# Optimization experiments

Hardware: AMD Instinct MI355X
Metric: run time of the kernel (lower is better)

Reference implementation:

```python
import jax, jax.numpy as jnp
import numpy as np

H = 16        # num heads
NOPE = 128    # qk_nope_head_dim
ROPE = 64     # qk_rope_head_dim
VD = 128      # v_head_dim
HID = 2048    # hidden_dim
QLR = 1536    # q_lora_rank
KVLR = 512    # kv_lora_rank
B = 4
S = 1024
EPS = 1e-6


def setup_inputs() -> dict:
    key = jax.random.key(0)
    ks = jax.random.split(key, 8)
    def w(k, o, i):
        return jax.random.normal(k, (o, i), jnp.float32) * 0.02
    x = jax.random.normal(ks[0], (B * S, HID), jnp.float32)
    wq_a = w(ks[1], QLR, HID)
    w_qa_ln = jnp.ones((QLR,), jnp.float32)
    wq_b = w(ks[2], H * (NOPE + ROPE), QLR)
    wkv_a = w(ks[3], KVLR + ROPE, HID)
    w_kva_ln = jnp.ones((KVLR,), jnp.float32)
    wk_b = w(ks[4], H * NOPE, KVLR)
    wv_b = w(ks[5], H * VD, KVLR)
    wo = w(ks[6], HID, H * VD)
    # interleaved RoPE tables: [S, ROPE//2]
    pos = jnp.arange(S, dtype=jnp.float32)
    inv_freq = 1.0 / (10000.0 ** (jnp.arange(0, ROPE, 2, dtype=jnp.float32) / ROPE))
    freqs = pos[:, None] * inv_freq[None, :]
    rotary_sin = jnp.sin(freqs)
    rotary_cos = jnp.cos(freqs)
    seqstarts = jnp.arange(B + 1, dtype=jnp.int32) * S
    return dict(x=x, wq_a=wq_a, w_qa_ln=w_qa_ln, wq_b=wq_b, wkv_a=wkv_a,
                w_kva_ln=w_kva_ln, wk_b=wk_b, wv_b=wv_b, wo=wo,
                rotary_sin=rotary_sin, rotary_cos=rotary_cos, seqstarts=seqstarts)


def rmsnorm(h, w):
    return h * jax.lax.rsqrt(jnp.mean(h * h, axis=-1, keepdims=True) + EPS) * w


def rope_interleaved(t, sin, cos):
    # t: [B,S,h,ROPE]; sin/cos: [S,ROPE//2]; rotate adjacent pairs (even, odd)
    tr = t.reshape(t.shape[:-1] + (ROPE // 2, 2))
    e, o = tr[..., 0], tr[..., 1]
    s = sin[None, :, None, :]
    c = cos[None, :, None, :]
    return jnp.stack([e * c - o * s, e * s + o * c], axis=-1).reshape(t.shape)


def reference(x, wq_a, w_qa_ln, wq_b, wkv_a, w_kva_ln, wk_b, wv_b, wo,
              rotary_sin, rotary_cos, seqstarts):
    b = seqstarts.shape[0] - 1
    s = x.shape[0] // b
    # low-rank Q: hidden -> q_lora -> H*(nope+rope)
    q = rmsnorm(x @ wq_a.T, w_qa_ln) @ wq_b.T
    q = q.reshape(b, s, H, NOPE + ROPE)
    q_nope, q_pe = q[..., :NOPE], q[..., NOPE:]
    # low-rank KV: hidden -> kv_lora + rope (k_pe shared across heads)
    kv = x @ wkv_a.T
    ckv = rmsnorm(kv[:, :KVLR], w_kva_ln)
    k_pe = kv[:, KVLR:].reshape(b, s, 1, ROPE)
    k_nope = (ckv @ wk_b.T).reshape(b, s, H, NOPE)
    v = (ckv @ wv_b.T).reshape(b, s, H, VD)
    q_pe = rope_interleaved(q_pe, rotary_sin, rotary_cos)
    k_pe = rope_interleaved(k_pe, rotary_sin, rotary_cos)
    scale = 1.0 / np.sqrt(NOPE + ROPE).astype(np.float32)
    scores = (jnp.einsum('bqhd,bkhd->bhqk', q_nope, k_nope)
              + jnp.einsum('bqhd,bkjd->bhqk', q_pe, k_pe)) * scale
    causal = jnp.tril(jnp.ones((s, s), bool))
    scores = jnp.where(causal[None, None], scores, jnp.float32(-1e30))
    p = jax.nn.softmax(scores, axis=-1)
    out = jnp.einsum('bhqk,bkhd->bqhd', p, v).reshape(b * s, H * VD)
    return out @ wo.T
```

## Files before the change

### kernel.cpp

```cpp
#include <hip/hip_runtime.h>
#include <stdint.h>

typedef __bf16 bf16;
typedef __bf16 bf16x8 __attribute__((ext_vector_type(8)));
typedef float floatx4 __attribute__((ext_vector_type(4)));
typedef float floatx16 __attribute__((ext_vector_type(16)));

#define HH     16
#define DNOPE  128
#define DROPE  64
#define DV     128
#define DQK    192
#define HID    2048
#define QLR    1536
#define KVLR   512
#define BB     4
#define SS     1024
#define NTOK   4096
#define XOUTW  2176
#define EPSF   1e-6f

__device__ inline void cvt_store4(bf16* dst, float a, float b, float c, float d) {
  union { bf16 h[4]; uint2 u; } t;
  t.h[0] = (bf16)a; t.h[1] = (bf16)b; t.h[2] = (bf16)c; t.h[3] = (bf16)d;
  *(uint2*)dst = t.u;
}

__device__ inline void gl_lds16(const bf16* g, bf16* l) {
  __builtin_amdgcn_global_load_lds(
      (const __attribute__((address_space(1))) void*)g,
      (__attribute__((address_space(3))) void*)l, 16, 0, 0);
}

__global__ __launch_bounds__(256) void cvt_all(
    const float* __restrict__ x, const float* __restrict__ wq_a,
    const float* __restrict__ wkv_a, const float* __restrict__ wq_b,
    const float* __restrict__ wk_b, const float* __restrict__ wv_b,
    const float* __restrict__ wo, bf16* __restrict__ xb,
    bf16* __restrict__ wA, bf16* __restrict__ wqbb,
    bf16* __restrict__ wkvB, bf16* __restrict__ wob, float scaleq) {
  const int blk = blockIdx.x, tid = threadIdx.x;
  const float* s; bf16* d; int rel; float sc = 1.0f;
  if (blk < 8192)       { rel = blk;         s = x;    d = xb; }
  else if (blk < 11264) { rel = blk - 8192;  s = wq_a; d = wA; }
  else if (blk < 12544) {
    rel = blk - 11264;
    int i = (rel * 256 + tid) << 2;
    bf16* dd = wA + 3145728;
    if ((i >> 11) < 576) {
      float4 v = *(const float4*)(wkv_a + i);
      cvt_store4(dd + i, v.x, v.y, v.z, v.w);
    } else {
      *(uint2*)(dd + i) = make_uint2(0u, 0u);
    }
    return;
  }
  else if (blk < 17152) { rel = blk - 12544; s = wq_b; d = wqbb; sc = scaleq; }
  else if (blk < 18176) { rel = blk - 17152; s = wk_b; d = wkvB; }
  else if (blk < 19200) { rel = blk - 18176; s = wv_b; d = wkvB + 1048576; }
  else                  { rel = blk - 19200; s = wo;   d = wob; }
  int i = (rel * 256 + tid) << 2;
  float4 v = *(const float4*)(s + i);
  cvt_store4(d + i, v.x * sc, v.y * sc, v.z * sc, v.w * sc);
}

template <typename TC, int EPI>
__global__ __launch_bounds__(256) void gemm_bt_bf16(
    const bf16* __restrict__ A, const bf16* __restrict__ Bw,
    TC* __restrict__ C0, bf16* __restrict__ C1, int M, int N, int K) {
  __shared__ __align__(16) bf16 As[128 * 64];
  __shared__ __align__(16) bf16 Bs[128 * 64];
  const int tid  = threadIdx.x;
  const int wave = tid >> 6, lane = tid & 63;
  const int m0 = blockIdx.x << 7, n0 = blockIdx.y << 7;
  const int quad = lane >> 4, l16 = lane & 15;
  const int wm = (wave >> 1) << 6, wn = (wave & 1) << 6;
  const int srow = wave << 5;
  const int lrow = lane >> 3;
  const int lcol = (lane & 7) << 3;

  const bf16* gA = A  + (size_t)(m0 + srow + lrow) * K + lcol;
  const bf16* gB = Bw + (size_t)(n0 + srow + lrow) * K + lcol;
  bf16* lA = As + srow * 64;
  bf16* lB = Bs + srow * 64;

  floatx4 acc[4][4];
#pragma unroll
  for (int i = 0; i < 4; i++)
#pragma unroll
    for (int j = 0; j < 4; j++) acc[i][j] = floatx4{0.f, 0.f, 0.f, 0.f};

  for (int k0 = 0; k0 < K; k0 += 64) {
    __syncthreads();
#pragma unroll
    for (int t = 0; t < 4; t++) {
      gl_lds16(gA + (size_t)(t << 3) * K + k0, lA + (t << 3) * 64);
      gl_lds16(gB + (size_t)(t << 3) * K + k0, lB + (t << 3) * 64);
    }
    __syncthreads();
#pragma unroll
    for (int ks = 0; ks < 2; ks++) {
      bf16x8 af[4], bv[4];
#pragma unroll
      for (int i = 0; i < 4; i++)
        af[i] = *(const bf16x8*)&As[(wm + (i << 4) + l16) * 64 + (ks << 5) + (quad << 3)];
#pragma unroll
      for (int j = 0; j < 4; j++)
        bv[j] = *(const bf16x8*)&Bs[(wn + (j << 4) + l16) * 64 + (ks << 5) + (quad << 3)];
#pragma unroll
      for (int i = 0; i < 4; i++)
#pragma unroll
        for (int j = 0; j < 4; j++)
          acc[i][j] = __builtin_amdgcn_mfma_f32_16x16x32_bf16(af[i], bv[j], acc[i][j], 0, 0, 0);
    }
  }

  if constexpr (EPI == 1) {
    if (n0 >= 2048) {
#pragma unroll
      for (int i = 0; i < 4; i++) {
        int gm = m0 + wm + (i << 4) + (quad << 2);
        int bb = gm >> 10, s = gm & 1023;
#pragma unroll
        for (int j = 0; j < 4; j++) {
          int gn = n0 + wn + (j << 4) + l16 - 2048;
          int hh = gn >> 7, vd = gn & 127;
          union { bf16 h4[4]; uint2 u; } pk;
#pragma unroll
          for (int r = 0; r < 4; r++) pk.h4[r] = (bf16)acc[i][j][r];
          *(uint2*)(C1 + ((((size_t)bb * HH + hh) * DV + vd) << 10) + s) = pk.u;
        }
      }
      return;
    }
  }
  const int ldc = (EPI == 1) ? 2048 : N;
#pragma unroll
  for (int i = 0; i < 4; i++)
#pragma unroll
    for (int j = 0; j < 4; j++) {
      int gn = n0 + wn + (j << 4) + l16;
#pragma unroll
      for (int r = 0; r < 4; r++) {
        int gm = m0 + wm + (i << 4) + (quad << 2) + r;
        C0[(size_t)gm * ldc + gn] = (TC)acc[i][j][r];
      }
    }
}

__global__ __launch_bounds__(256) void norm_rope(
    const bf16* __restrict__ xout, const float* __restrict__ w_qa_ln,
    const float* __restrict__ w_kva_ln, bf16* __restrict__ qln,
    bf16* __restrict__ ckv, bf16* __restrict__ kpe,
    const float* __restrict__ rsin, const float* __restrict__ rcos) {
  const int blk = blockIdx.x, tid = threadIdx.x;
  if (blk < 8192) {
    const int row = blk & 4095;
    const bool isq = blk < 4096;
    const bf16* p = xout + (size_t)row * XOUTW + (isq ? 0 : QLR);
    const float* w = isq ? w_qa_ln : w_kva_ln;
    bf16* o = isq ? (qln + (size_t)row * QLR) : (ckv + (size_t)row * KVLR);
    const int L = isq ? QLR : KVLR;
    float ss = 0.f;
    for (int c = tid << 2; c < L; c += 1024) {
      union { uint2 u; bf16 h[4]; } t;
      t.u = *(const uint2*)(p + c);
#pragma unroll
      for (int r = 0; r < 4; r++) { float v = (float)t.h[r]; ss += v * v; }
    }
#pragma unroll
    for (int off = 32; off > 0; off >>= 1) ss += __shfl_down(ss, off);
    __shared__ float red[4];
    if ((tid & 63) == 0) red[tid >> 6] = ss;
    __syncthreads();
    float rs = rsqrtf((red[0] + red[1] + red[2] + red[3]) / (float)L + EPSF);
    for (int c = tid << 2; c < L; c += 1024) {
      union { uint2 u; bf16 h[4]; } t, ot;
      t.u = *(const uint2*)(p + c);
#pragma unroll
      for (int r = 0; r < 4; r++) ot.h[r] = (bf16)((float)t.h[r] * rs * w[c + r]);
      *(uint2*)(o + c) = ot.u;
    }
  } else {
    int idx = (blk - 8192) * 256 + tid;
    int i = idx & 31, row = idx >> 5;
    int pos = row & (SS - 1);
    union { uint u; bf16 h2[2]; } t;
    t.u = *(const uint*)(xout + (size_t)row * XOUTW + QLR + KVLR + (i << 1));
    float e = (float)t.h2[0], o = (float)t.h2[1];
    float c = rcos[(pos << 5) + i], s = rsin[(pos << 5) + i];
    t.h2[0] = (bf16)(e * c - o * s);
    t.h2[1] = (bf16)(e * s + o * c);
    *(uint*)(kpe + (size_t)row * DROPE + (i << 1)) = t.u;
  }
}

__global__ void rope_q(bf16* __restrict__ q, const float* __restrict__ sin_t,
                       const float* __restrict__ cos_t) {
  int idx = blockIdx.x * 256 + threadIdx.x;
  int i = idx & 31, h = (idx >> 5) & 15, row = idx >> 9;
  int pos = row & (SS - 1);
  bf16* base = q + ((size_t)row * HH + h) * DQK + DNOPE + (i << 1);
  union { uint u; bf16 h2[2]; } t;
  t.u = *(uint*)base;
  float e = (float)t.h2[0], o = (float)t.h2[1];
  float c = cos_t[(pos << 5) + i], s = sin_t[(pos << 5) + i];
  t.h2[0] = (bf16)(e * c - o * s);
  t.h2[1] = (bf16)(e * s + o * c);
  *(uint*)base = t.u;
}

__global__ __launch_bounds__(512, 2) void attn_kernel(
    const bf16* __restrict__ q, const bf16* __restrict__ knope,
    const bf16* __restrict__ kpe, const bf16* __restrict__ vT,
    bf16* __restrict__ out) {
  const int qt = 3 - blockIdx.x;
  const int q0 = qt << 8;
  const int nkt = (qt + 1) << 2;
  const int h = blockIdx.y, b = blockIdx.z;
  __shared__ __align__(16) bf16 smem[40960];
  const int tid = threadIdx.x, wave = tid >> 6, lane = tid & 63;
  const int l32 = lane & 31, hi = lane >> 5;
  const int hi4 = hi << 2;
  const int Q0w = q0 + (wave << 5);
  const int qg = Q0w + l32;

  const bf16 *gkn0, *gkn1, *gkp, *gvt0, *gvt1;
  {
    int c = wave << 1;
    int r = (c << 2) + (lane >> 4);
    int bi = (lane & 15) ^ (r & 15);
    gkn0 = knope + ((size_t)((b << 10) + r) * HH + h) * DNOPE + (bi << 3);
    r = ((c + 1) << 2) + (lane >> 4);
    bi = (lane & 15) ^ (r & 15);
    gkn1 = knope + ((size_t)((b << 10) + r) * HH + h) * DNOPE + (bi << 3);
    r = (wave << 3) + (lane >> 3);
    bi = (lane & 7) ^ (r & 7);
    gkp = kpe + (size_t)((b << 10) + r) * DROPE + (bi << 3);
    int dv = (wave << 4) + (lane >> 3);
    bi = (lane & 7) ^ (dv & 7);
    gvt0 = vT + ((((size_t)b * HH + h) * DV + dv) << 10) + (bi << 3);
    dv += 8;
    bi = (lane & 7) ^ (dv & 7);
    gvt1 = vT + ((((size_t)b * HH + h) * DV + dv) << 10) + (bi << 3);
  }
  const size_t knstep = (size_t)64 * HH * DNOPE;
  const size_t kpstep = (size_t)64 * DROPE;
  const int woff = wave << 10, woff2 = wave << 9;

  gl_lds16(gkn0, smem + woff);
  gl_lds16(gkn1, smem + woff + 512);
  gl_lds16(gkp,  smem + 8192 + woff2);
  gl_lds16(gvt0, smem + 12288 + woff);
  gl_lds16(gvt1, smem + 12288 + woff + 512);
  gkn0 += knstep; gkn1 += knstep; gkp += kpstep; gvt0 += 64; gvt1 += 64;

  bf16x8 qb[12];
  {
    const bf16* qbase =
        q + ((size_t)((b << 10) + Q0w + l32) * HH + h) * DQK + (hi << 3);
#pragma unroll
    for (int dc = 0; dc < 12; dc++)
      qb[dc] = *(const bf16x8*)(qbase + (dc << 4));
  }

  floatx16 acc[4];
#pragma unroll
  for (int g = 0; g < 4; g++)
#pragma unroll
    for (int r = 0; r < 16; r++) acc[g][r] = 0.f;
  float m_i = -1e30f, l_i = 0.f;

  for (int s = 0; s < nkt; s++) {
    const int k0 = s << 6;
    asm volatile("s_waitcnt vmcnt(0)\n\ts_barrier" ::: "memory");
    if (s + 1 < nkt) {
      bf16* bufp = smem + ((s + 1) & 1) * 20480;
      gl_lds16(gkn0, bufp + woff);
      gl_lds16(gkn1, bufp + woff + 512);
      gl_lds16(gkp,  bufp + 8192 + woff2);
      gl_lds16(gvt0, bufp + 12288 + woff);
      gl_lds16(gvt1, bufp + 12288 + woff + 512);
      gkn0 += knstep; gkn1 += knstep; gkp += kpstep; gvt0 += 64; gvt1 += 64;
    }
    __builtin_amdgcn_sched_barrier(0);
    if (k0 > Q0w + 31) continue;

    const bf16* Kn = smem + (s & 1) * 20480;
    const bf16* Kp = Kn + 8192;
    const bf16* Vt = Kn + 12288;

    floatx16 s0, s1;
#pragma unroll
    for (int r = 0; r < 16; r++) { s0[r] = 0.f; s1[r] = 0.f; }
    __builtin_amdgcn_s_setprio(1);
#pragma unroll
    for (int dc = 0; dc < 12; dc++) {
      bf16x8 ak0, ak1;
      if (dc < 8) {
        int gi = (((dc << 1) + hi) ^ (l32 & 15)) << 3;
        ak0 = *(const bf16x8*)&Kn[(l32 << 7) + gi];
        ak1 = *(const bf16x8*)&Kn[((32 + l32) << 7) + gi];
      } else {
        int gi = ((((dc - 8) << 1) + hi) ^ (l32 & 7)) << 3;
        ak0 = *(const bf16x8*)&Kp[(l32 << 6) + gi];
        ak1 = *(const bf16x8*)&Kp[((32 + l32) << 6) + gi];
      }
      s0 = __builtin_amdgcn_mfma_f32_32x32x16_bf16(ak0, qb[dc], s0, 0, 0, 0);
      s1 = __builtin_amdgcn_mfma_f32_32x32x16_bf16(ak1, qb[dc], s1, 0, 0, 0);
    }
    __builtin_amdgcn_s_setprio(0);

    if (k0 + 63 > Q0w) {
#pragma unroll
      for (int r = 0; r < 16; r++) {
        int rp = (r & 3) + ((r >> 2) << 3) + hi4;
        if (k0 + rp > qg)      s0[r] = -1e30f;
        if (k0 + 32 + rp > qg) s1[r] = -1e30f;
      }
    }

    float mx = -1e30f;
#pragma unroll
    for (int r = 0; r < 16; r++) mx = fmaxf(mx, fmaxf(s0[r], s1[r]));
    mx = fmaxf(mx, __shfl_xor(mx, 32));
    if (!__all(mx - m_i <= 8.0f)) {
      float mnew = fmaxf(m_i, mx);
      float alpha = exp2f(m_i - mnew);
      l_i *= alpha;
#pragma unroll
      for (int g = 0; g < 4; g++)
#pragma unroll
        for (int r = 0; r < 16; r++) acc[g][r] *= alpha;
      m_i = mnew;
    }
    float sum = 0.f;
#pragma unroll
    for (int r = 0; r < 16; r++) {
      float p0 = exp2f(s0[r] - m_i), p1 = exp2f(s1[r] - m_i);
      s0[r] = p0; s1[r] = p1;
      sum += p0 + p1;
    }
    sum += __shfl_xor(sum, 32);
    l_i += sum;

    uint P32[2][4][2];
#pragma unroll
    for (int hh = 0; hh < 4; hh++) {
      union { bf16 e[2]; uint u; } w0, w1, w2, w3;
      w0.e[0] = (bf16)s0[(hh << 2) + 0]; w0.e[1] = (bf16)s0[(hh << 2) + 1];
      w1.e[0] = (bf16)s0[(hh << 2) + 2]; w1.e[1] = (bf16)s0[(hh << 2) + 3];
      w2.e[0] = (bf16)s1[(hh << 2) + 0]; w2.e[1] = (bf16)s1[(hh << 2) + 1];
      w3.e[0] = (bf16)s1[(hh << 2) + 2]; w3.e[1] = (bf16)s1[(hh << 2) + 3];
      P32[0][hh][0] = w0.u; P32[0][hh][1] = w1.u;
      P32[1][hh][0] = w2.u; P32[1][hh][1] = w3.u;
    }
    bf16x8 bp[4];
#pragma unroll
    for (int c = 0; c < 4; c++) {
      const int t = c >> 1, sb = c & 1;
      uint send0 = hi ? P32[t][(sb << 1)][0] : P32[t][(sb << 1) + 1][0];
      uint send1 = hi ? P32[t][(sb << 1)][1] : P32[t][(sb << 1) + 1][1];
      uint r0 = __shfl_xor(send0, 32);
      uint r1 = __shfl_xor(send1, 32);
      union { uint u[4]; bf16x8 v; } f;
      if (hi == 0) {
        f.u[0] = P32[t][(sb << 1)][0]; f.u[1] = P32[t][(sb << 1)][1];
        f.u[2] = r0;                   f.u[3] = r1;
      } else {
        f.u[0] = r0;                         f.u[1] = r1;
        f.u[2] = P32[t][(sb << 1) + 1][0];   f.u[3] = P32[t][(sb << 1) + 1][1];
      }
      bp[c] = f.v;
    }

    __builtin_amdgcn_s_setprio(1);
#pragma unroll
    for (int c = 0; c < 4; c++) {
      const int gsw = (((c << 1) + hi) ^ (l32 & 7)) << 3;
#pragma unroll
      for (int g = 0; g < 4; g++) {
        bf16x8 av = *(const bf16x8*)&Vt[(((g << 5) + l32) << 6) + gsw];
        acc[g] = __builtin_amdgcn_mfma_f32_32x32x16_bf16(av, bp[c], acc[g], 0, 0, 0);
      }
    }
    __builtin_amdgcn_s_setprio(0);
  }

  const float invl = 1.0f / l_i;
  const int tok = (b << 10) + Q0w + l32;
  bf16* obase = out + ((size_t)tok * HH + h) * DV + hi4;
#pragma unroll
  for (int g = 0; g < 4; g++)
#pragma unroll
    for (int t = 0; t < 4; t++) {
      union { bf16 h4[4]; uint2 u; } pk;
#pragma unroll
      for (int r = 0; r < 4; r++)
        pk.h4[r] = (bf16)(acc[g][(t << 2) + r] * invl);
      *(uint2*)(obase + (g << 5) + (t << 3)) = pk.u;
    }
}

extern "C" void kernel_launch(void* const* d_in, const int* in_sizes, int n_in,
                              void* d_out, int out_size, void* d_ws, size_t ws_size,
                              hipStream_t stream) {
  (void)in_sizes; (void)n_in; (void)out_size; (void)ws_size;
  const float* x        = (const float*)d_in[0];
  const float* wq_a     = (const float*)d_in[1];
  const float* w_qa_ln  = (const float*)d_in[2];
  const float* wq_b     = (const float*)d_in[3];
  const float* wkv_a    = (const float*)d_in[4];
  const float* w_kva_ln = (const float*)d_in[5];
  const float* wk_b     = (const float*)d_in[6];
  const float* wv_b     = (const float*)d_in[7];
  const float* wo       = (const float*)d_in[8];
  const float* rsin     = (const float*)d_in[9];
  const float* rcos     = (const float*)d_in[10];
  float* out = (float*)d_out;

  char* ws = (char*)d_ws;
  bf16* xb    = (bf16*)(ws + 0);
  bf16* attnb = (bf16*)(ws + 0);
  bf16* xout  = (bf16*)(ws + 16777216);
  bf16* knope = (bf16*)(ws + 16777216);
  bf16* q     = (bf16*)(ws + 34603008);
  bf16* qln   = (bf16*)(ws + 59768832);
  bf16* vT    = (bf16*)(ws + 59768832);
  bf16* wA    = (bf16*)(ws + 76546048);
  bf16* wqbb  = (bf16*)(ws + 85458944);
  bf16* wkvB  = (bf16*)(ws + 94896128);
  bf16* wob   = (bf16*)(ws + 99090432);
  bf16* ckv   = (bf16*)(ws + 107479040);
  bf16* kpe   = (bf16*)(ws + 111673344);

  const float SCALEQ = (1.0f / sqrtf(192.0f)) * 1.44269504088896f;

  dim3 blk(256);
  cvt_all<<<23296, blk, 0, stream>>>(x, wq_a, wkv_a, wq_b, wk_b, wv_b, wo,
                                     xb, wA, wqbb, wkvB, wob, SCALEQ);
  gemm_bt_bf16<bf16, 0><<<dim3(32, 17), blk, 0, stream>>>(
      xb, wA, xout, nullptr, NTOK, XOUTW, HID);
  norm_rope<<<8704, blk, 0, stream>>>(xout, w_qa_ln, w_kva_ln, qln, ckv, kpe,
                                      rsin, rcos);
  gemm_bt_bf16<bf16, 0><<<dim3(32, 24), blk, 0, stream>>>(
      qln, wqbb, q, nullptr, NTOK, HH * DQK, QLR);
  rope_q<<<8192, blk, 0, stream>>>(q, rsin, rcos);
  gemm_bt_bf16<bf16, 1><<<dim3(32, 32), blk, 0, stream>>>(
      ckv, wkvB, knope, vT, NTOK, 4096, KVLR);
  attn_kernel<<<dim3(4, HH, BB), dim3(512), 0, stream>>>(
      q, knope, kpe, vT, attnb);
  gemm_bt_bf16<float, 0><<<dim3(32, 16), blk, 0, stream>>>(
      attnb, wob, out, nullptr, NTOK, HID, HID);
}
```

Before: 452.8 us.

## Double-buffer LDS tiles in bf16 GEMM to overlap global loads with MFMA

The GEMM kernel now keeps two LDS buffers for the A and B tiles. It prefetches the next K-tile with direct global-to-LDS loads while the MFMAs run on the current tile, and replaces the two barriers per iteration with a single waitcnt+barrier. The goal is to hide global memory latency that the old load-sync-compute loop exposed. In exchange, LDS use per block doubles, which may lower occupancy, and correctness depends on the wave-uniform LDS base handling in gl_lds16.

```diff
diff --git a/kernel.cpp b/kernel.cpp
--- a/kernel.cpp
+++ b/kernel.cpp
@@ -68,8 +68,8 @@
 __global__ __launch_bounds__(256) void gemm_bt_bf16(
     const bf16* __restrict__ A, const bf16* __restrict__ Bw,
     TC* __restrict__ C0, bf16* __restrict__ C1, int M, int N, int K) {
-  __shared__ __align__(16) bf16 As[128 * 64];
-  __shared__ __align__(16) bf16 Bs[128 * 64];
+  __shared__ __align__(16) bf16 As[2][128 * 64];
+  __shared__ __align__(16) bf16 Bs[2][128 * 64];
   const int tid  = threadIdx.x;
   const int wave = tid >> 6, lane = tid & 63;
   const int m0 = blockIdx.x << 7, n0 = blockIdx.y << 7;
@@ -81,8 +81,7 @@
 
   const bf16* gA = A  + (size_t)(m0 + srow + lrow) * K + lcol;
   const bf16* gB = Bw + (size_t)(n0 + srow + lrow) * K + lcol;
-  bf16* lA = As + srow * 64;
-  bf16* lB = Bs + srow * 64;
+  const int soff = (srow + lrow) * 64;
 
   floatx4 acc[4][4];
 #pragma unroll
@@ -90,23 +89,38 @@
 #pragma unroll
     for (int j = 0; j < 4; j++) acc[i][j] = floatx4{0.f, 0.f, 0.f, 0.f};
 
-  for (int k0 = 0; k0 < K; k0 += 64) {
-    __syncthreads();
-#pragma unroll
-    for (int t = 0; t < 4; t++) {
-      gl_lds16(gA + (size_t)(t << 3) * K + k0, lA + (t << 3) * 64);
-      gl_lds16(gB + (size_t)(t << 3) * K + k0, lB + (t << 3) * 64);
-    }
-    __syncthreads();
+#pragma unroll
+  for (int t = 0; t < 4; t++) {
+    gl_lds16(gA + (size_t)(t << 3) * K, As[0] + soff + (t << 3) * 64);
+    gl_lds16(gB + (size_t)(t << 3) * K, Bs[0] + soff + (t << 3) * 64);
+  }
+
+  const int nk = K >> 6;
+  for (int kt = 0; kt < nk; kt++) {
+    asm volatile("s_waitcnt vmcnt(0)\n\ts_barrier" ::: "memory");
+    if (kt + 1 < nk) {
+      const int kn = (kt + 1) << 6;
+      bf16* lA = As[(kt + 1) & 1] + soff;
+      bf16* lB = Bs[(kt + 1) & 1] + soff;
+#pragma unroll
+      for (int t = 0; t < 4; t++) {
+        gl_lds16(gA + (size_t)(t << 3) * K + kn, lA + (t << 3) * 64);
+        gl_lds16(gB + (size_t)(t << 3) * K + kn, lB + (t << 3) * 64);
+      }
+    }
+    __builtin_amdgcn_sched_barrier(0);
+
+    const bf16* cA = As[kt & 1];
+    const bf16* cB = Bs[kt & 1];
 #pragma unroll
     for (int ks = 0; ks < 2; ks++) {
       bf16x8 af[4], bv[4];
 #pragma unroll
       for (int i = 0; i < 4; i++)
-        af[i] = *(const bf16x8*)&As[(wm + (i << 4) + l16) * 64 + (ks << 5) + (quad << 3)];
+        af[i] = *(const bf16x8*)&cA[(wm + (i << 4) + l16) * 64 + (ks << 5) + (quad << 3)];
 #pragma unroll
       for (int j = 0; j < 4; j++)
-        bv[j] = *(const bf16x8*)&Bs[(wn + (j << 4) + l16) * 64 + (ks << 5) + (quad << 3)];
+        bv[j] = *(const bf16x8*)&cB[(wn + (j << 4) + l16) * 64 + (ks << 5) + (quad << 3)];
 #pragma unroll
       for (int i = 0; i < 4; i++)
 #pragma unroll
```

Measured after the change: 438.3 us. 1.03x faster.
